# Kernel optimization log

Measured on AMD Instinct MI355X. Metric: run time of the kernel, lower is better.

The kernel has to match this reference:

```python
import jax, jax.numpy as jnp
import numpy as np

ALPHA = 0.5
SMOOTH = 1e-05
ITERS = 10


def _max_pool3x3(x):
    # 3x3 max pool, stride 1, SAME padding on NCHW tensor
    return jax.lax.reduce_window(
        x, -jnp.inf, jax.lax.max,
        window_dimensions=(1, 1, 3, 3),
        window_strides=(1, 1, 1, 1),
        padding='SAME')


def _soft_erode(x):
    return -_max_pool3x3(-x)


def _soft_dilate(x):
    return _max_pool3x3(x)


def _soft_skeletonize(img, iterations=ITERS):
    def body(skel, _):
        eroded = _soft_erode(skel)
        temp = _soft_dilate(eroded)
        skel = skel - (skel - eroded) * temp
        skel = jnp.clip(skel, 0.0, 1.0)
        return skel, None
    skel, _ = jax.lax.scan(body, img, None, length=iterations)
    return skel


def _dice_score(pred, target, smooth=SMOOTH):
    inter = jnp.sum(pred * target, axis=(2, 3))
    union = jnp.sum(pred, axis=(2, 3)) + jnp.sum(target, axis=(2, 3))
    dice = (2.0 * inter + smooth) / (union + smooth)
    return jnp.mean(dice)


def setup_inputs() -> dict:
    key = jax.random.key(0)
    k1, k2 = jax.random.split(key)
    B, C, H, W = 32, 1, 512, 512
    pred_logits = jax.random.normal(k1, (B, C, H, W), dtype=jnp.float32)
    target = jax.random.uniform(k2, (B, C, H, W), dtype=jnp.float32)
    return {"pred_logits": pred_logits, "target": target}


def reference(pred_logits, target):
    pred = jax.nn.sigmoid(pred_logits)
    dice = _dice_score(pred, target)
    pred_skel = _soft_skeletonize(pred)
    target_skel = _soft_skeletonize(target)
    skel_dice = _dice_score(pred_skel, target_skel)
    loss = (1.0 - ALPHA) * (1.0 - dice) + ALPHA * (1.0 - skel_dice)
    return (loss, dice, skel_dice)
```

## Files before the change

kernel.cpp:

```cpp
#include <hip/hip_runtime.h>
#include <hip/hip_fp16.h>
#include <math.h>


#define H 512
#define W 512
#define IMG (H * W)
#define NIMG 64
#define NPRED 32

#define APU 72
#define AROWS 74
#define BPU 68
#define BROWS 68
#define TQ 17
#define S1ITEMS 238
#define FILLN (AROWS * 18)

#define PINF2 0x7C007C00u
#define NINF2 0xFC00FC00u
#define ONE2  0x3C003C00u

typedef _Float16 f16;
typedef _Float16 h2 __attribute__((ext_vector_type(2)));
typedef __fp16 fp16v2 __attribute__((ext_vector_type(2)));

__device__ __forceinline__ float2 unpack2(uint u) {
    fp16v2 h = __builtin_bit_cast(fp16v2, u);
    return make_float2((float)h.x, (float)h.y);
}
__device__ __forceinline__ uint pack2(float a, float b) {
    fp16v2 h = __builtin_amdgcn_cvt_pkrtz(a, b);
    return __builtin_bit_cast(uint, h);
}
__device__ __forceinline__ uint pmin(uint a, uint b) {
    uint d; asm("v_pk_min_f16 %0, %1, %2" : "=v"(d) : "v"(a), "v"(b)); return d;
}
__device__ __forceinline__ uint pmax(uint a, uint b) {
    uint d; asm("v_pk_max_f16 %0, %1, %2" : "=v"(d) : "v"(a), "v"(b)); return d;
}
__device__ __forceinline__ uint abit(uint hi, uint lo) {
    return __builtin_amdgcn_alignbit(hi, lo, 16);
}

__device__ __forceinline__ void lds_dma16(uint* l, const void* g) {
    __builtin_amdgcn_global_load_lds(
        (__attribute__((address_space(1))) void*)(g),
        (__attribute__((address_space(3))) void*)(l), 16, 0, 0);
}

__device__ __forceinline__ float wsum64(float v) {
#pragma unroll
    for (int o = 32; o > 0; o >>= 1) v += __shfl_down(v, o);
    return v;
}

__device__ __forceinline__ void hmin8p(const uint* __restrict__ p, uint m[6], uint sc[4]) {
    uint4 w0 = *(const uint4*)(p);
    uint4 w1 = *(const uint4*)(p + 4);
    uint w[8] = {w0.x, w0.y, w0.z, w0.w, w1.x, w1.y, w1.z, w1.w};
    sc[0] = w[2]; sc[1] = w[3]; sc[2] = w[4]; sc[3] = w[5];
    uint s[7];
#pragma unroll
    for (int j = 0; j < 7; j++) s[j] = abit(w[j + 1], w[j]);
#pragma unroll
    for (int i = 0; i < 6; i++) m[i] = pmin(s[i], pmin(w[i + 1], s[i + 1]));
}

template<bool EDGE>
__device__ __forceinline__ void erode8(const uint a[6], const uint b[6], const uint c[6],
                                       bool rowok, const bool* eok, uint e[6]) {
#pragma unroll
    for (int i = 0; i < 6; i++) {
        uint v = pmin(a[i], pmin(b[i], c[i]));
        e[i] = EDGE ? ((rowok && eok[i]) ? v : NINF2) : v;
    }
}

__device__ __forceinline__ void hmax8(const uint e[6], uint hx[4], uint ec[4]) {
    uint a[5];
#pragma unroll
    for (int j = 0; j < 5; j++) a[j] = abit(e[j + 1], e[j]);
#pragma unroll
    for (int p = 0; p < 4; p++) {
        hx[p] = pmax(a[p], pmax(e[p + 1], a[p + 1]));
        ec[p] = e[p + 1];
    }
}

__device__ __forceinline__ uint upd_pair(uint s, uint ec, uint t) {
    h2 sh = __builtin_bit_cast(h2, s);
    h2 eh = __builtin_bit_cast(h2, ec);
    h2 th = __builtin_bit_cast(h2, t);
    h2 o = sh - (sh - eh) * th;
    return pmin(pmax(__builtin_bit_cast(uint, o), 0u), ONE2);
}

template<bool EDGE, int SIG>
__device__ float2 fillA_f32(uint* __restrict__ A, const float* __restrict__ src,
                            const float* __restrict__ tgt,
                            int tileX, int tileY, int tid) {
    float a = 0.0f, b = 0.0f;
#pragma unroll
    for (int hf = 0; hf < 2; hf++) {
        float4 v0[3], v1[3], t0[3], t1[3];
        bool ld[3];
#pragma unroll
        for (int j = 0; j < 3; j++) {
            const int i = tid + 256 * (3 * hf + j);
            const int r = i / 18;
            const int q = i - 18 * r;
            const int gy = tileY + r - 4;
            const int gx = tileX - 8 + 8 * q;
            bool ok = (i < FILLN);
            if (EDGE) ok = ok && (r < 72) && ((unsigned)gy < (unsigned)H) &&
                           ((unsigned)gx < (unsigned)W);
            ld[j] = ok;
            if (ok) {
                const float* sp = src + (size_t)gy * W + gx;
                v0[j] = *(const float4*)(sp);
                v1[j] = *(const float4*)(sp + 4);
                if (SIG) {
                    const float* tp = tgt + (size_t)gy * W + gx;
                    t0[j] = *(const float4*)(tp);
                    t1[j] = *(const float4*)(tp + 4);
                }
            }
        }
#pragma unroll
        for (int j = 0; j < 3; j++) {
            const int i = tid + 256 * (3 * hf + j);
            const int r = i / 18;
            const int q = i - 18 * r;
            if (i < FILLN) {
                uint4 w = make_uint4(PINF2, PINF2, PINF2, PINF2);
                if (ld[j]) {
                    float4 f0 = v0[j], f1 = v1[j];
                    if (SIG) {
                        f0.x = 1.0f / (1.0f + __expf(-f0.x));
                        f0.y = 1.0f / (1.0f + __expf(-f0.y));
                        f0.z = 1.0f / (1.0f + __expf(-f0.z));
                        f0.w = 1.0f / (1.0f + __expf(-f0.w));
                        f1.x = 1.0f / (1.0f + __expf(-f1.x));
                        f1.y = 1.0f / (1.0f + __expf(-f1.y));
                        f1.z = 1.0f / (1.0f + __expf(-f1.z));
                        f1.w = 1.0f / (1.0f + __expf(-f1.w));
                    }
                    if (((unsigned)(r - 4) < 64u) && ((unsigned)(q - 1) < 16u)) {
                        if (SIG) {
                            a += f0.x * t0[j].x + f0.y * t0[j].y + f0.z * t0[j].z +
                                 f0.w * t0[j].w + f1.x * t1[j].x + f1.y * t1[j].y +
                                 f1.z * t1[j].z + f1.w * t1[j].w;
                            b += f0.x + f0.y + f0.z + f0.w + f1.x + f1.y + f1.z + f1.w;
                        } else {
                            a += f0.x + f0.y + f0.z + f0.w + f1.x + f1.y + f1.z + f1.w;
                        }
                    }
                    w.x = pack2(f0.x, f0.y); w.y = pack2(f0.z, f0.w);
                    w.z = pack2(f1.x, f1.y); w.w = pack2(f1.z, f1.w);
                }
                *(uint4*)(A + r * APU + 4 * q) = w;
            }
        }
    }
    return make_float2(a, b);
}

__device__ __forceinline__ void fill_dma(uint* __restrict__ A, const f16* __restrict__ src,
                                         int tileX, int tileY, int tid) {
#pragma unroll
    for (int j = 0; j < 6; j++) {
        const int i = tid + 256 * j;
        if (i < FILLN) {
            const int r = i / 18;
            const int q = i - 18 * r;
            const int gy = tileY + r - 4;
            const int gx = tileX - 8 + 8 * q;
            if (gx < 0 || gx >= W) {
                *(uint4*)(A + 4 * i) = make_uint4(PINF2, PINF2, PINF2, PINF2);
            } else {
                const int gyc = min(max(gy, 0), H - 1);
                lds_dma16(A + 4 * i, src + (size_t)gyc * W + gx);
            }
        }
    }
}

template<bool EDGE>
__device__ void stage1(const uint* __restrict__ Au, uint* __restrict__ Bu,
                       int tileX, int tileY, int tid) {
    if (tid >= S1ITEMS) return;
    const int s = tid / TQ;
    const int g = tid - TQ * s;
    const int gcb = tileX + 8 * g - 4;
    const int ys = tileY - 2 + 5 * s;
    bool eok[6], wok[4];
    if (EDGE) {
#pragma unroll
        for (int i = 0; i < 6; i++) eok[i] = ((unsigned)(gcb - 2 + 2 * i) < (unsigned)W);
#pragma unroll
        for (int p = 0; p < 4; p++) wok[p] = ((unsigned)(gcb + 2 * p) < (unsigned)W);
    }
    const int lr = 5 * s + 2;
    const uint* Ab = Au + 4 * g;
    uint m[3][6], sc[3][4], hx[3][4], e[6], ec_cur[4], ec_nxt[4], tsc[4];
    hmin8p(Ab + (lr - 2) * APU, m[0], tsc);
    hmin8p(Ab + (lr - 1) * APU, m[1], tsc);
    hmin8p(Ab + (lr + 0) * APU, m[2], sc[0]);
    erode8<EDGE>(m[0], m[1], m[2], (unsigned)(ys - 1) < (unsigned)H, eok, e);
    hmax8(e, hx[0], ec_nxt);
    hmin8p(Ab + (lr + 1) * APU, m[0], sc[1]);
    erode8<EDGE>(m[1], m[2], m[0], (unsigned)ys < (unsigned)H, eok, e);
    hmax8(e, hx[1], ec_cur);
#pragma unroll
    for (int k = 0; k < 5; k++) {
        hmin8p(Ab + (lr + 2 + k) * APU, m[(k + 1) % 3], sc[(2 + k) % 3]);
        erode8<EDGE>(m[(k + 2) % 3], m[k % 3], m[(k + 1) % 3],
                     (unsigned)(ys + k + 1) < (unsigned)H, eok, e);
        hmax8(e, hx[(k + 2) % 3], ec_nxt);
        const int br = 5 * s + k;
        if (br < BROWS) {
            const bool rin = EDGE ? ((unsigned)(ys + k) < (unsigned)H) : true;
            uint o[4];
#pragma unroll
            for (int p = 0; p < 4; p++) {
                uint t = pmax(hx[k % 3][p], pmax(hx[(k + 1) % 3][p], hx[(k + 2) % 3][p]));
                uint v = upd_pair(sc[k % 3][p], ec_cur[p], t);
                o[p] = EDGE ? ((rin && wok[p]) ? v : PINF2) : v;
            }
            *(uint4*)(Bu + br * BPU + 4 * g) = make_uint4(o[0], o[1], o[2], o[3]);
        }
#pragma unroll
        for (int p = 0; p < 4; p++) ec_cur[p] = ec_nxt[p];
    }
}

template<bool EDGE, bool TOREG>
__device__ void stage2(const uint* __restrict__ Bu, int tileX, int tileY, int tid,
                       f16* __restrict__ gdst, uint* __restrict__ oreg) {
    const int g = tid & 15;
    const int ty = tid >> 4;
    const int X = tileX + 8 * g;
    const int gy0 = tileY + 4 * ty;
    const int rb = 4 * ty + 2;
    bool eok[6];
    if (EDGE) {
#pragma unroll
        for (int i = 0; i < 6; i++) eok[i] = ((unsigned)(X - 2 + 2 * i) < (unsigned)W);
    }
    const uint* Bb = Bu + 4 * g;
    uint m[3][6], sc[3][4], hx[3][4], e[6], ec_cur[4], ec_nxt[4], tsc[4];
    hmin8p(Bb + (rb - 2) * BPU, m[0], tsc);
    hmin8p(Bb + (rb - 1) * BPU, m[1], tsc);
    hmin8p(Bb + (rb + 0) * BPU, m[2], sc[0]);
    erode8<EDGE>(m[0], m[1], m[2], (unsigned)(gy0 - 1) < (unsigned)H, eok, e);
    hmax8(e, hx[0], ec_nxt);
    hmin8p(Bb + (rb + 1) * BPU, m[0], sc[1]);
    erode8<EDGE>(m[1], m[2], m[0], true, eok, e);
    hmax8(e, hx[1], ec_cur);
#pragma unroll
    for (int k = 0; k < 4; k++) {
        hmin8p(Bb + (rb + 2 + k) * BPU, m[(k + 1) % 3], sc[(2 + k) % 3]);
        erode8<EDGE>(m[(k + 2) % 3], m[k % 3], m[(k + 1) % 3],
                     (unsigned)(gy0 + k + 1) < (unsigned)H, eok, e);
        hmax8(e, hx[(k + 2) % 3], ec_nxt);
        uint o[4];
#pragma unroll
        for (int p = 0; p < 4; p++) {
            uint t = pmax(hx[k % 3][p], pmax(hx[(k + 1) % 3][p], hx[(k + 2) % 3][p]));
            o[p] = upd_pair(sc[k % 3][p], ec_cur[p], t);
        }
        if (TOREG) {
#pragma unroll
            for (int p = 0; p < 4; p++) oreg[4 * k + p] = o[p];
        } else {
            *(uint4*)(gdst + (size_t)(gy0 + k) * W + X) = make_uint4(o[0], o[1], o[2], o[3]);
        }
#pragma unroll
        for (int p = 0; p < 4; p++) ec_cur[p] = ec_nxt[p];
    }
}

__device__ __forceinline__ bool is_edge() {
    return (blockIdx.x == 0) | (blockIdx.x == 3) | (blockIdx.y == 0) | (blockIdx.y == 7);
}

__global__ __launch_bounds__(256, 4) void k_first(
    const float* __restrict__ logits, const float* __restrict__ target,
    f16* __restrict__ outb, float* __restrict__ parts0, float* __restrict__ parts1) {
    __shared__ __align__(16) uint A[AROWS * APU];
    __shared__ __align__(16) uint Bu[BROWS * BPU];
    __shared__ float red[8];
    const int img = blockIdx.z;
    const int tileX = blockIdx.x * 128, tileY = blockIdx.y * 64;
    const int tid = threadIdx.x;
    const bool pred = (img < NPRED);
    const bool edge = is_edge();
    float2 ab;
    if (edge) {
        if (pred) ab = fillA_f32<true, 1>(A, logits + (size_t)img * IMG,
                                          target + (size_t)img * IMG, tileX, tileY, tid);
        else      ab = fillA_f32<true, 0>(A, target + (size_t)(img - NPRED) * IMG,
                                          nullptr, tileX, tileY, tid);
    } else {
        if (pred) ab = fillA_f32<false, 1>(A, logits + (size_t)img * IMG,
                                           target + (size_t)img * IMG, tileX, tileY, tid);
        else      ab = fillA_f32<false, 0>(A, target + (size_t)(img - NPRED) * IMG,
                                           nullptr, tileX, tileY, tid);
    }
    __syncthreads();
    float a = wsum64(ab.x), b = wsum64(ab.y);
    if ((tid & 63) == 0) { red[tid >> 6] = a; red[4 + (tid >> 6)] = b; }
    if (edge) stage1<true>(A, Bu, tileX, tileY, tid);
    else      stage1<false>(A, Bu, tileX, tileY, tid);
    __syncthreads();
    if (tid == 0) {
        int bi = blockIdx.z * 32 + blockIdx.y * 4 + blockIdx.x;
        parts0[bi] = red[0] + red[1] + red[2] + red[3];
        parts1[bi] = red[4] + red[5] + red[6] + red[7];
    }
    if (edge) stage2<true, false>(Bu, tileX, tileY, tid, outb + (size_t)img * IMG, nullptr);
    else      stage2<false, false>(Bu, tileX, tileY, tid, outb + (size_t)img * IMG, nullptr);
}

__global__ __launch_bounds__(256, 4) void k_mid(
    const f16* __restrict__ in, f16* __restrict__ outb) {
    __shared__ __align__(16) uint A[AROWS * APU];
    __shared__ __align__(16) uint Bu[BROWS * BPU];
    const int img = blockIdx.z;
    const int tileX = blockIdx.x * 128, tileY = blockIdx.y * 64;
    const int tid = threadIdx.x;
    const bool edge = is_edge();
    fill_dma(A, in + (size_t)img * IMG, tileX, tileY, tid);
    __syncthreads();
    if (edge) {
        stage1<true>(A, Bu, tileX, tileY, tid);
        __syncthreads();
        stage2<true, false>(Bu, tileX, tileY, tid, outb + (size_t)img * IMG, nullptr);
    } else {
        stage1<false>(A, Bu, tileX, tileY, tid);
        __syncthreads();
        stage2<false, false>(Bu, tileX, tileY, tid, outb + (size_t)img * IMG, nullptr);
    }
}

__global__ __launch_bounds__(256, 4) void k_last(
    const f16* __restrict__ in, float* __restrict__ pA,
    float* __restrict__ pB, float* __restrict__ pC) {
    __shared__ __align__(16) uint A[AROWS * APU];
    __shared__ __align__(16) uint Bu[BROWS * BPU];
    __shared__ float red[12];
    const int img = blockIdx.z;
    const int tileX = blockIdx.x * 128, tileY = blockIdx.y * 64;
    const int tid = threadIdx.x;
    const bool edge = is_edge();
    uint op[16], ot[16];
    fill_dma(A, in + (size_t)img * IMG, tileX, tileY, tid);
    __syncthreads();
    if (edge) {
        stage1<true>(A, Bu, tileX, tileY, tid);
        __syncthreads();
        stage2<true, true>(Bu, tileX, tileY, tid, nullptr, op);
        fill_dma(A, in + (size_t)(img + NPRED) * IMG, tileX, tileY, tid);
        __syncthreads();
        stage1<true>(A, Bu, tileX, tileY, tid);
        __syncthreads();
        stage2<true, true>(Bu, tileX, tileY, tid, nullptr, ot);
    } else {
        stage1<false>(A, Bu, tileX, tileY, tid);
        __syncthreads();
        stage2<false, true>(Bu, tileX, tileY, tid, nullptr, op);
        fill_dma(A, in + (size_t)(img + NPRED) * IMG, tileX, tileY, tid);
        __syncthreads();
        stage1<false>(A, Bu, tileX, tileY, tid);
        __syncthreads();
        stage2<false, true>(Bu, tileX, tileY, tid, nullptr, ot);
    }
    float a = 0.0f, b = 0.0f, c = 0.0f;
#pragma unroll
    for (int j = 0; j < 16; j++) {
        float2 p = unpack2(op[j]);
        float2 t = unpack2(ot[j]);
        a += p.x * t.x + p.y * t.y;
        b += p.x + p.y;
        c += t.x + t.y;
    }
    a = wsum64(a); b = wsum64(b); c = wsum64(c);
    if ((tid & 63) == 0) {
        red[tid >> 6] = a; red[4 + (tid >> 6)] = b; red[8 + (tid >> 6)] = c;
    }
    __syncthreads();
    if (tid == 0) {
        int bi = img * 32 + blockIdx.y * 4 + blockIdx.x;
        pA[bi] = red[0] + red[1] + red[2] + red[3];
        pB[bi] = red[4] + red[5] + red[6] + red[7];
        pC[bi] = red[8] + red[9] + red[10] + red[11];
    }
}

__global__ __launch_bounds__(64) void finalize_img(
    const float* __restrict__ parts0, const float* __restrict__ parts1,
    const float* __restrict__ pA, const float* __restrict__ pB,
    const float* __restrict__ pC, float* __restrict__ dices) {
    const int i = blockIdx.x, t = threadIdx.x;
    const bool v = (t < 32);
    float inter = wsum64(v ? parts0[i * 32 + t] : 0.0f);
    float sp = wsum64(v ? parts1[i * 32 + t] : 0.0f);
    float st = wsum64(v ? parts0[(NPRED + i) * 32 + t] : 0.0f);
    float i2 = wsum64(v ? pA[i * 32 + t] : 0.0f);
    float sp2 = wsum64(v ? pB[i * 32 + t] : 0.0f);
    float st2 = wsum64(v ? pC[i * 32 + t] : 0.0f);
    if (t == 0) {
        dices[i] = (float)((2.0 * (double)inter + 1e-5) / ((double)sp + (double)st + 1e-5));
        dices[32 + i] = (float)((2.0 * (double)i2 + 1e-5) / ((double)sp2 + (double)st2 + 1e-5));
    }
}

__global__ void finalize_out(const float* __restrict__ dices, float* __restrict__ out) {
    const int t = threadIdx.x;
    double d = 0.0, sd = 0.0;
    if (t < 32) { d = dices[t]; sd = dices[32 + t]; }
#pragma unroll
    for (int o = 32; o > 0; o >>= 1) { d += __shfl_down(d, o); sd += __shfl_down(sd, o); }
    if (t == 0) {
        d *= (1.0 / 32.0); sd *= (1.0 / 32.0);
        out[0] = (float)(0.5 * (1.0 - d) + 0.5 * (1.0 - sd));
        out[1] = (float)d;
        out[2] = (float)sd;
    }
}

extern "C" void kernel_launch(void* const* d_in, const int* in_sizes, int n_in,
                              void* d_out, int out_size, void* d_ws, size_t ws_size,
                              hipStream_t stream) {
    (void)in_sizes; (void)n_in; (void)out_size; (void)ws_size;
    const float* logits = (const float*)d_in[0];
    const float* target = (const float*)d_in[1];
    float* out = (float*)d_out;
    f16* buf0 = (f16*)d_ws;
    f16* buf1 = buf0 + (size_t)NIMG * IMG;
    float* parts0 = (float*)(buf1 + (size_t)NIMG * IMG);
    float* parts1 = parts0 + 2048;
    float* pA = parts1 + 2048;
    float* pB = pA + 1024;
    float* pC = pB + 1024;
    float* dices = pC + 1024;

    dim3 blk(256, 1, 1);
    k_first<<<dim3(4, 8, NIMG), blk, 0, stream>>>(logits, target, buf0, parts0, parts1);
    k_mid<<<dim3(4, 8, NIMG), blk, 0, stream>>>(buf0, buf1);
    k_mid<<<dim3(4, 8, NIMG), blk, 0, stream>>>(buf1, buf0);
    k_mid<<<dim3(4, 8, NIMG), blk, 0, stream>>>(buf0, buf1);
    k_last<<<dim3(4, 8, NPRED), blk, 0, stream>>>(buf1, pA, pB, pC);
    finalize_img<<<32, 64, 0, stream>>>(parts0, parts1, pA, pB, pC, dices);
    finalize_out<<<1, 64, 0, stream>>>(dices, out);
}
```

Before: 220.0 us.

## Process two row tiles per k_mid block and overlap next DMA fill with stage2

k_mid now handles two vertically adjacent tiles per block, with the grid halved in y. The second tile's shared-memory fill is issued before the first tile's stage2 so the load overlaps compute. k_last likewise prefetches the target image's tile during the pred tile's stage2. This is meant to hide global load latency, at the cost of fewer blocks (less parallelism) in k_mid and a dependence on fill_dma being asynchronous with respect to stage2's reads of Bu only.

```diff
diff --git a/kernel.cpp b/kernel.cpp
--- a/kernel.cpp
+++ b/kernel.cpp
@@ -281,10 +281,6 @@
     }
 }
 
-__device__ __forceinline__ bool is_edge() {
-    return (blockIdx.x == 0) | (blockIdx.x == 3) | (blockIdx.y == 0) | (blockIdx.y == 7);
-}
-
 __global__ __launch_bounds__(256, 4) void k_first(
     const float* __restrict__ logits, const float* __restrict__ target,
     f16* __restrict__ outb, float* __restrict__ parts0, float* __restrict__ parts1) {
@@ -295,7 +291,8 @@
     const int tileX = blockIdx.x * 128, tileY = blockIdx.y * 64;
     const int tid = threadIdx.x;
     const bool pred = (img < NPRED);
-    const bool edge = is_edge();
+    const bool edge = (blockIdx.x == 0) | (blockIdx.x == 3) |
+                      (blockIdx.y == 0) | (blockIdx.y == 7);
     float2 ab;
     if (edge) {
         if (pred) ab = fillA_f32<true, 1>(A, logits + (size_t)img * IMG,
@@ -328,20 +325,30 @@
     __shared__ __align__(16) uint A[AROWS * APU];
     __shared__ __align__(16) uint Bu[BROWS * BPU];
     const int img = blockIdx.z;
-    const int tileX = blockIdx.x * 128, tileY = blockIdx.y * 64;
+    const int tileX = blockIdx.x * 128;
+    const int by0 = blockIdx.y * 2;
+    const int tY0 = by0 * 64, tY1 = tY0 + 64;
     const int tid = threadIdx.x;
-    const bool edge = is_edge();
-    fill_dma(A, in + (size_t)img * IMG, tileX, tileY, tid);
-    __syncthreads();
-    if (edge) {
-        stage1<true>(A, Bu, tileX, tileY, tid);
-        __syncthreads();
-        stage2<true, false>(Bu, tileX, tileY, tid, outb + (size_t)img * IMG, nullptr);
-    } else {
-        stage1<false>(A, Bu, tileX, tileY, tid);
-        __syncthreads();
-        stage2<false, false>(Bu, tileX, tileY, tid, outb + (size_t)img * IMG, nullptr);
-    }
+    const f16* src = in + (size_t)img * IMG;
+    f16* dst = outb + (size_t)img * IMG;
+    const bool ex = (blockIdx.x == 0) | (blockIdx.x == 3);
+    const bool e0 = ex | (by0 == 0);
+    const bool e1 = ex | (by0 + 1 == 7);
+
+    fill_dma(A, src, tileX, tY0, tid);
+    __syncthreads();
+    if (e0) stage1<true>(A, Bu, tileX, tY0, tid);
+    else    stage1<false>(A, Bu, tileX, tY0, tid);
+    __syncthreads();
+    fill_dma(A, src, tileX, tY1, tid);
+    if (e0) stage2<true, false>(Bu, tileX, tY0, tid, dst, nullptr);
+    else    stage2<false, false>(Bu, tileX, tY0, tid, dst, nullptr);
+    __syncthreads();
+    if (e1) stage1<true>(A, Bu, tileX, tY1, tid);
+    else    stage1<false>(A, Bu, tileX, tY1, tid);
+    __syncthreads();
+    if (e1) stage2<true, false>(Bu, tileX, tY1, tid, dst, nullptr);
+    else    stage2<false, false>(Bu, tileX, tY1, tid, dst, nullptr);
 }
 
 __global__ __launch_bounds__(256, 4) void k_last(
@@ -353,29 +360,23 @@
     const int img = blockIdx.z;
     const int tileX = blockIdx.x * 128, tileY = blockIdx.y * 64;
     const int tid = threadIdx.x;
-    const bool edge = is_edge();
+    const bool edge = (blockIdx.x == 0) | (blockIdx.x == 3) |
+                      (blockIdx.y == 0) | (blockIdx.y == 7);
     uint op[16], ot[16];
     fill_dma(A, in + (size_t)img * IMG, tileX, tileY, tid);
     __syncthreads();
-    if (edge) {
-        stage1<true>(A, Bu, tileX, tileY, tid);
-        __syncthreads();
-        stage2<true, true>(Bu, tileX, tileY, tid, nullptr, op);
-        fill_dma(A, in + (size_t)(img + NPRED) * IMG, tileX, tileY, tid);
-        __syncthreads();
-        stage1<true>(A, Bu, tileX, tileY, tid);
-        __syncthreads();
-        stage2<true, true>(Bu, tileX, tileY, tid, nullptr, ot);
-    } else {
-        stage1<false>(A, Bu, tileX, tileY, tid);
-        __syncthreads();
-        stage2<false, true>(Bu, tileX, tileY, tid, nullptr, op);
-        fill_dma(A, in + (size_t)(img + NPRED) * IMG, tileX, tileY, tid);
-        __syncthreads();
-        stage1<false>(A, Bu, tileX, tileY, tid);
-        __syncthreads();
-        stage2<false, true>(Bu, tileX, tileY, tid, nullptr, ot);
-    }
+    if (edge) stage1<true>(A, Bu, tileX, tileY, tid);
+    else      stage1<false>(A, Bu, tileX, tileY, tid);
+    __syncthreads();
+    fill_dma(A, in + (size_t)(img + NPRED) * IMG, tileX, tileY, tid);
+    if (edge) stage2<true, true>(Bu, tileX, tileY, tid, nullptr, op);
+    else      stage2<false, true>(Bu, tileX, tileY, tid, nullptr, op);
+    __syncthreads();
+    if (edge) stage1<true>(A, Bu, tileX, tileY, tid);
+    else      stage1<false>(A, Bu, tileX, tileY, tid);
+    __syncthreads();
+    if (edge) stage2<true, true>(Bu, tileX, tileY, tid, nullptr, ot);
+    else      stage2<false, true>(Bu, tileX, tileY, tid, nullptr, ot);
     float a = 0.0f, b = 0.0f, c = 0.0f;
 #pragma unroll
     for (int j = 0; j < 16; j++) {
@@ -448,9 +449,9 @@
 
     dim3 blk(256, 1, 1);
     k_first<<<dim3(4, 8, NIMG), blk, 0, stream>>>(logits, target, buf0, parts0, parts1);
-    k_mid<<<dim3(4, 8, NIMG), blk, 0, stream>>>(buf0, buf1);
-    k_mid<<<dim3(4, 8, NIMG), blk, 0, stream>>>(buf1, buf0);
-    k_mid<<<dim3(4, 8, NIMG), blk, 0, stream>>>(buf0, buf1);
+    k_mid<<<dim3(4, 4, NIMG), blk, 0, stream>>>(buf0, buf1);
+    k_mid<<<dim3(4, 4, NIMG), blk, 0, stream>>>(buf1, buf0);
+    k_mid<<<dim3(4, 4, NIMG), blk, 0, stream>>>(buf0, buf1);
     k_last<<<dim3(4, 8, NPRED), blk, 0, stream>>>(buf1, pA, pB, pC);
     finalize_img<<<32, 64, 0, stream>>>(parts0, parts1, pA, pB, pC, dices);
     finalize_out<<<1, 64, 0, stream>>>(dices, out);
```

Measured after the change: 222.7 us. Within noise of the previous version (+1.2%).

## Fuse four skeletonize iterations per kernel with wider halo tiles

Applied to the files above, without the earlier changes.

Replaces the three two-iteration mid kernels and the two-iteration last kernel with kernels that each run four skeleton iterations in shared memory. They use a wider halo (8 rows and 16 columns) and ping-pong between two LDS buffers. This removes two kernel launches and their global f16 round trips, at the cost of redundant halo compute, more LDS per block and lower occupancy (launch bounds 3). The last kernel also prefetches the target tile into LDS during the final stage of the pred chain.

```diff
diff --git a/kernel.cpp b/kernel.cpp
--- a/kernel.cpp
+++ b/kernel.cpp
@@ -11,11 +11,13 @@
 
 #define APU 72
 #define AROWS 74
-#define BPU 68
-#define BROWS 68
-#define TQ 17
-#define S1ITEMS 238
 #define FILLN (AROWS * 18)
+#define DPU 68
+#define A4P 80
+#define A4R 82
+#define B4P 76
+#define C4P 72
+#define FILL4N 1600
 
 #define PINF2 0x7C007C00u
 #define NINF2 0xFC00FC00u
@@ -94,6 +96,101 @@
     h2 th = __builtin_bit_cast(h2, t);
     h2 o = sh - (sh - eh) * th;
     return pmin(pmax(__builtin_bit_cast(uint, o), 0u), ONE2);
+}
+
+template<bool EDGE, int PIN, int POUT, int NG, int NSTRIP, int SROWS, int NROWS, int RO>
+__device__ void stageN(const uint* __restrict__ in, uint* __restrict__ out,
+                       int tileX, int tileY, int tid) {
+    if (tid >= NSTRIP * NG) return;
+    const int s = tid / NG;
+    const int g = tid - NG * s;
+    const int c0 = tileX - 2 * RO + 8 * g;
+    const int ys = tileY + SROWS * s - RO;
+    bool eok[6], wok[4];
+    if (EDGE) {
+#pragma unroll
+        for (int i = 0; i < 6; i++) eok[i] = ((unsigned)(c0 - 2 + 2 * i) < (unsigned)W);
+#pragma unroll
+        for (int p = 0; p < 4; p++) wok[p] = ((unsigned)(c0 + 2 * p) < (unsigned)W);
+    }
+    const int lr = SROWS * s + 2;
+    const uint* Ab = in + 4 * g;
+    uint m[3][6], sc[3][4], hx[3][4], e[6], ec_cur[4], ec_nxt[4], tsc[4];
+    hmin8p(Ab + (lr - 2) * PIN, m[0], tsc);
+    hmin8p(Ab + (lr - 1) * PIN, m[1], tsc);
+    hmin8p(Ab + (lr + 0) * PIN, m[2], sc[0]);
+    erode8<EDGE>(m[0], m[1], m[2], (unsigned)(ys - 1) < (unsigned)H, eok, e);
+    hmax8(e, hx[0], ec_nxt);
+    hmin8p(Ab + (lr + 1) * PIN, m[0], sc[1]);
+    erode8<EDGE>(m[1], m[2], m[0], (unsigned)ys < (unsigned)H, eok, e);
+    hmax8(e, hx[1], ec_cur);
+#pragma unroll
+    for (int k = 0; k < SROWS; k++) {
+        hmin8p(Ab + (lr + 2 + k) * PIN, m[(k + 1) % 3], sc[(2 + k) % 3]);
+        erode8<EDGE>(m[(k + 2) % 3], m[k % 3], m[(k + 1) % 3],
+                     (unsigned)(ys + k + 1) < (unsigned)H, eok, e);
+        hmax8(e, hx[(k + 2) % 3], ec_nxt);
+        const int br = SROWS * s + k;
+        if (NSTRIP * SROWS <= NROWS || br < NROWS) {
+            const bool rin = EDGE ? ((unsigned)(ys + k) < (unsigned)H) : true;
+            uint o[4];
+#pragma unroll
+            for (int p = 0; p < 4; p++) {
+                uint t = pmax(hx[k % 3][p], pmax(hx[(k + 1) % 3][p], hx[(k + 2) % 3][p]));
+                uint v = upd_pair(sc[k % 3][p], ec_cur[p], t);
+                o[p] = EDGE ? ((rin && wok[p]) ? v : PINF2) : v;
+            }
+            *(uint4*)(out + br * POUT + 4 * g) = make_uint4(o[0], o[1], o[2], o[3]);
+        }
+#pragma unroll
+        for (int p = 0; p < 4; p++) ec_cur[p] = ec_nxt[p];
+    }
+}
+
+template<bool EDGE, bool TOREG>
+__device__ void stage2(const uint* __restrict__ Du, int tileX, int tileY, int tid,
+                       f16* __restrict__ gdst, uint* __restrict__ oreg) {
+    const int g = tid & 15;
+    const int ty = tid >> 4;
+    const int X = tileX + 8 * g;
+    const int gy0 = tileY + 4 * ty;
+    const int rb = 4 * ty + 2;
+    bool eok[6];
+    if (EDGE) {
+#pragma unroll
+        for (int i = 0; i < 6; i++) eok[i] = ((unsigned)(X - 2 + 2 * i) < (unsigned)W);
+    }
+    const uint* Bb = Du + 4 * g;
+    uint m[3][6], sc[3][4], hx[3][4], e[6], ec_cur[4], ec_nxt[4], tsc[4];
+    hmin8p(Bb + (rb - 2) * DPU, m[0], tsc);
+    hmin8p(Bb + (rb - 1) * DPU, m[1], tsc);
+    hmin8p(Bb + (rb + 0) * DPU, m[2], sc[0]);
+    erode8<EDGE>(m[0], m[1], m[2], (unsigned)(gy0 - 1) < (unsigned)H, eok, e);
+    hmax8(e, hx[0], ec_nxt);
+    hmin8p(Bb + (rb + 1) * DPU, m[0], sc[1]);
+    erode8<EDGE>(m[1], m[2], m[0], true, eok, e);
+    hmax8(e, hx[1], ec_cur);
+#pragma unroll
+    for (int k = 0; k < 4; k++) {
+        hmin8p(Bb + (rb + 2 + k) * DPU, m[(k + 1) % 3], sc[(2 + k) % 3]);
+        erode8<EDGE>(m[(k + 2) % 3], m[k % 3], m[(k + 1) % 3],
+                     (unsigned)(gy0 + k + 1) < (unsigned)H, eok, e);
+        hmax8(e, hx[(k + 2) % 3], ec_nxt);
+        uint o[4];
+#pragma unroll
+        for (int p = 0; p < 4; p++) {
+            uint t = pmax(hx[k % 3][p], pmax(hx[(k + 1) % 3][p], hx[(k + 2) % 3][p]));
+            o[p] = upd_pair(sc[k % 3][p], ec_cur[p], t);
+        }
+        if (TOREG) {
+#pragma unroll
+            for (int p = 0; p < 4; p++) oreg[4 * k + p] = o[p];
+        } else {
+            *(uint4*)(gdst + (size_t)(gy0 + k) * W + X) = make_uint4(o[0], o[1], o[2], o[3]);
+        }
+#pragma unroll
+        for (int p = 0; p < 4; p++) ec_cur[p] = ec_nxt[p];
+    }
 }
 
 template<bool EDGE, int SIG>
@@ -166,119 +263,39 @@
     return make_float2(a, b);
 }
 
-__device__ __forceinline__ void fill_dma(uint* __restrict__ A, const f16* __restrict__ src,
-                                         int tileX, int tileY, int tid) {
-#pragma unroll
-    for (int j = 0; j < 6; j++) {
+__device__ __forceinline__ void fill_dma4(uint* __restrict__ A, const f16* __restrict__ src,
+                                          int tileX, int tileY, int tid) {
+#pragma unroll
+    for (int j = 0; j < 7; j++) {
         const int i = tid + 256 * j;
-        if (i < FILLN) {
-            const int r = i / 18;
-            const int q = i - 18 * r;
-            const int gy = tileY + r - 4;
-            const int gx = tileX - 8 + 8 * q;
+        if (i < FILL4N) {
+            const int r = i / 20;
+            const int q = i - 20 * r;
+            const int gy = tileY + r - 8;
+            const int gx = tileX - 16 + 8 * q;
             if (gx < 0 || gx >= W) {
-                *(uint4*)(A + 4 * i) = make_uint4(PINF2, PINF2, PINF2, PINF2);
+                *(uint4*)(A + r * A4P + 4 * q) = make_uint4(PINF2, PINF2, PINF2, PINF2);
             } else {
                 const int gyc = min(max(gy, 0), H - 1);
-                lds_dma16(A + 4 * i, src + (size_t)gyc * W + gx);
+                lds_dma16(A + r * A4P + 4 * q, src + (size_t)gyc * W + gx);
             }
         }
     }
 }
 
-template<bool EDGE>
-__device__ void stage1(const uint* __restrict__ Au, uint* __restrict__ Bu,
-                       int tileX, int tileY, int tid) {
-    if (tid >= S1ITEMS) return;
-    const int s = tid / TQ;
-    const int g = tid - TQ * s;
-    const int gcb = tileX + 8 * g - 4;
-    const int ys = tileY - 2 + 5 * s;
-    bool eok[6], wok[4];
-    if (EDGE) {
-#pragma unroll
-        for (int i = 0; i < 6; i++) eok[i] = ((unsigned)(gcb - 2 + 2 * i) < (unsigned)W);
-#pragma unroll
-        for (int p = 0; p < 4; p++) wok[p] = ((unsigned)(gcb + 2 * p) < (unsigned)W);
-    }
-    const int lr = 5 * s + 2;
-    const uint* Ab = Au + 4 * g;
-    uint m[3][6], sc[3][4], hx[3][4], e[6], ec_cur[4], ec_nxt[4], tsc[4];
-    hmin8p(Ab + (lr - 2) * APU, m[0], tsc);
-    hmin8p(Ab + (lr - 1) * APU, m[1], tsc);
-    hmin8p(Ab + (lr + 0) * APU, m[2], sc[0]);
-    erode8<EDGE>(m[0], m[1], m[2], (unsigned)(ys - 1) < (unsigned)H, eok, e);
-    hmax8(e, hx[0], ec_nxt);
-    hmin8p(Ab + (lr + 1) * APU, m[0], sc[1]);
-    erode8<EDGE>(m[1], m[2], m[0], (unsigned)ys < (unsigned)H, eok, e);
-    hmax8(e, hx[1], ec_cur);
-#pragma unroll
-    for (int k = 0; k < 5; k++) {
-        hmin8p(Ab + (lr + 2 + k) * APU, m[(k + 1) % 3], sc[(2 + k) % 3]);
-        erode8<EDGE>(m[(k + 2) % 3], m[k % 3], m[(k + 1) % 3],
-                     (unsigned)(ys + k + 1) < (unsigned)H, eok, e);
-        hmax8(e, hx[(k + 2) % 3], ec_nxt);
-        const int br = 5 * s + k;
-        if (br < BROWS) {
-            const bool rin = EDGE ? ((unsigned)(ys + k) < (unsigned)H) : true;
-            uint o[4];
-#pragma unroll
-            for (int p = 0; p < 4; p++) {
-                uint t = pmax(hx[k % 3][p], pmax(hx[(k + 1) % 3][p], hx[(k + 2) % 3][p]));
-                uint v = upd_pair(sc[k % 3][p], ec_cur[p], t);
-                o[p] = EDGE ? ((rin && wok[p]) ? v : PINF2) : v;
-            }
-            *(uint4*)(Bu + br * BPU + 4 * g) = make_uint4(o[0], o[1], o[2], o[3]);
-        }
-#pragma unroll
-        for (int p = 0; p < 4; p++) ec_cur[p] = ec_nxt[p];
-    }
-}
-
-template<bool EDGE, bool TOREG>
-__device__ void stage2(const uint* __restrict__ Bu, int tileX, int tileY, int tid,
-                       f16* __restrict__ gdst, uint* __restrict__ oreg) {
-    const int g = tid & 15;
-    const int ty = tid >> 4;
-    const int X = tileX + 8 * g;
-    const int gy0 = tileY + 4 * ty;
-    const int rb = 4 * ty + 2;
-    bool eok[6];
-    if (EDGE) {
-#pragma unroll
-        for (int i = 0; i < 6; i++) eok[i] = ((unsigned)(X - 2 + 2 * i) < (unsigned)W);
-    }
-    const uint* Bb = Bu + 4 * g;
-    uint m[3][6], sc[3][4], hx[3][4], e[6], ec_cur[4], ec_nxt[4], tsc[4];
-    hmin8p(Bb + (rb - 2) * BPU, m[0], tsc);
-    hmin8p(Bb + (rb - 1) * BPU, m[1], tsc);
-    hmin8p(Bb + (rb + 0) * BPU, m[2], sc[0]);
-    erode8<EDGE>(m[0], m[1], m[2], (unsigned)(gy0 - 1) < (unsigned)H, eok, e);
-    hmax8(e, hx[0], ec_nxt);
-    hmin8p(Bb + (rb + 1) * BPU, m[0], sc[1]);
-    erode8<EDGE>(m[1], m[2], m[0], true, eok, e);
-    hmax8(e, hx[1], ec_cur);
-#pragma unroll
-    for (int k = 0; k < 4; k++) {
-        hmin8p(Bb + (rb + 2 + k) * BPU, m[(k + 1) % 3], sc[(2 + k) % 3]);
-        erode8<EDGE>(m[(k + 2) % 3], m[k % 3], m[(k + 1) % 3],
-                     (unsigned)(gy0 + k + 1) < (unsigned)H, eok, e);
-        hmax8(e, hx[(k + 2) % 3], ec_nxt);
-        uint o[4];
-#pragma unroll
-        for (int p = 0; p < 4; p++) {
-            uint t = pmax(hx[k % 3][p], pmax(hx[(k + 1) % 3][p], hx[(k + 2) % 3][p]));
-            o[p] = upd_pair(sc[k % 3][p], ec_cur[p], t);
-        }
-        if (TOREG) {
-#pragma unroll
-            for (int p = 0; p < 4; p++) oreg[4 * k + p] = o[p];
-        } else {
-            *(uint4*)(gdst + (size_t)(gy0 + k) * W + X) = make_uint4(o[0], o[1], o[2], o[3]);
-        }
-#pragma unroll
-        for (int p = 0; p < 4; p++) ec_cur[p] = ec_nxt[p];
-    }
+template<bool EDGE, bool TOREG, bool PRE>
+__device__ void chain4(uint* __restrict__ A4, uint* __restrict__ B4,
+                       int tileX, int tileY, int tid,
+                       f16* __restrict__ dst, uint* __restrict__ oreg,
+                       const f16* __restrict__ pre) {
+    stageN<EDGE, A4P, B4P, 19, 13, 6, 76, 6>(A4, B4, tileX, tileY, tid);
+    __syncthreads();
+    stageN<EDGE, B4P, C4P, 18, 12, 6, 72, 4>(B4, A4, tileX, tileY, tid);
+    __syncthreads();
+    stageN<EDGE, C4P, DPU, 17, 14, 5, 68, 2>(A4, B4, tileX, tileY, tid);
+    __syncthreads();
+    if (PRE) fill_dma4(A4, pre, tileX, tileY, tid);
+    stage2<EDGE, TOREG>(B4, tileX, tileY, tid, dst, oreg);
 }
 
 __device__ __forceinline__ bool is_edge() {
@@ -289,7 +306,7 @@
     const float* __restrict__ logits, const float* __restrict__ target,
     f16* __restrict__ outb, float* __restrict__ parts0, float* __restrict__ parts1) {
     __shared__ __align__(16) uint A[AROWS * APU];
-    __shared__ __align__(16) uint Bu[BROWS * BPU];
+    __shared__ __align__(16) uint Bu[68 * DPU];
     __shared__ float red[8];
     const int img = blockIdx.z;
     const int tileX = blockIdx.x * 128, tileY = blockIdx.y * 64;
@@ -311,8 +328,8 @@
     __syncthreads();
     float a = wsum64(ab.x), b = wsum64(ab.y);
     if ((tid & 63) == 0) { red[tid >> 6] = a; red[4 + (tid >> 6)] = b; }
-    if (edge) stage1<true>(A, Bu, tileX, tileY, tid);
-    else      stage1<false>(A, Bu, tileX, tileY, tid);
+    if (edge) stageN<true, APU, DPU, 17, 14, 5, 68, 2>(A, Bu, tileX, tileY, tid);
+    else      stageN<false, APU, DPU, 17, 14, 5, 68, 2>(A, Bu, tileX, tileY, tid);
     __syncthreads();
     if (tid == 0) {
         int bi = blockIdx.z * 32 + blockIdx.y * 4 + blockIdx.x;
@@ -323,58 +340,44 @@
     else      stage2<false, false>(Bu, tileX, tileY, tid, outb + (size_t)img * IMG, nullptr);
 }
 
-__global__ __launch_bounds__(256, 4) void k_mid(
+__global__ __launch_bounds__(256, 3) void k_mid4(
     const f16* __restrict__ in, f16* __restrict__ outb) {
-    __shared__ __align__(16) uint A[AROWS * APU];
-    __shared__ __align__(16) uint Bu[BROWS * BPU];
+    __shared__ __align__(16) uint A4[A4R * A4P];
+    __shared__ __align__(16) uint B4[76 * B4P];
     const int img = blockIdx.z;
     const int tileX = blockIdx.x * 128, tileY = blockIdx.y * 64;
     const int tid = threadIdx.x;
     const bool edge = is_edge();
-    fill_dma(A, in + (size_t)img * IMG, tileX, tileY, tid);
-    __syncthreads();
-    if (edge) {
-        stage1<true>(A, Bu, tileX, tileY, tid);
-        __syncthreads();
-        stage2<true, false>(Bu, tileX, tileY, tid, outb + (size_t)img * IMG, nullptr);
-    } else {
-        stage1<false>(A, Bu, tileX, tileY, tid);
-        __syncthreads();
-        stage2<false, false>(Bu, tileX, tileY, tid, outb + (size_t)img * IMG, nullptr);
-    }
-}
-
-__global__ __launch_bounds__(256, 4) void k_last(
+    const f16* src = in + (size_t)img * IMG;
+    f16* dst = outb + (size_t)img * IMG;
+    fill_dma4(A4, src, tileX, tileY, tid);
+    __syncthreads();
+    if (edge) chain4<true, false, false>(A4, B4, tileX, tileY, tid, dst, nullptr, nullptr);
+    else      chain4<false, false, false>(A4, B4, tileX, tileY, tid, dst, nullptr, nullptr);
+}
+
+__global__ __launch_bounds__(256, 3) void k_last4(
     const f16* __restrict__ in, float* __restrict__ pA,
     float* __restrict__ pB, float* __restrict__ pC) {
-    __shared__ __align__(16) uint A[AROWS * APU];
-    __shared__ __align__(16) uint Bu[BROWS * BPU];
+    __shared__ __align__(16) uint A4[A4R * A4P];
+    __shared__ __align__(16) uint B4[76 * B4P];
     __shared__ float red[12];
     const int img = blockIdx.z;
     const int tileX = blockIdx.x * 128, tileY = blockIdx.y * 64;
     const int tid = threadIdx.x;
     const bool edge = is_edge();
     uint op[16], ot[16];
-    fill_dma(A, in + (size_t)img * IMG, tileX, tileY, tid);
+    const f16* tsrc = in + (size_t)(img + NPRED) * IMG;
+    fill_dma4(A4, in + (size_t)img * IMG, tileX, tileY, tid);
     __syncthreads();
     if (edge) {
-        stage1<true>(A, Bu, tileX, tileY, tid);
+        chain4<true, true, true>(A4, B4, tileX, tileY, tid, nullptr, op, tsrc);
         __syncthreads();
-        stage2<true, true>(Bu, tileX, tileY, tid, nullptr, op);
-        fill_dma(A, in + (size_t)(img + NPRED) * IMG, tileX, tileY, tid);
+        chain4<true, true, false>(A4, B4, tileX, tileY, tid, nullptr, ot, nullptr);
+    } else {
+        chain4<false, true, true>(A4, B4, tileX, tileY, tid, nullptr, op, tsrc);
         __syncthreads();
-        stage1<true>(A, Bu, tileX, tileY, tid);
-        __syncthreads();
-        stage2<true, true>(Bu, tileX, tileY, tid, nullptr, ot);
-    } else {
-        stage1<false>(A, Bu, tileX, tileY, tid);
-        __syncthreads();
-        stage2<false, true>(Bu, tileX, tileY, tid, nullptr, op);
-        fill_dma(A, in + (size_t)(img + NPRED) * IMG, tileX, tileY, tid);
-        __syncthreads();
-        stage1<false>(A, Bu, tileX, tileY, tid);
-        __syncthreads();
-        stage2<false, true>(Bu, tileX, tileY, tid, nullptr, ot);
+        chain4<false, true, false>(A4, B4, tileX, tileY, tid, nullptr, ot, nullptr);
     }
     float a = 0.0f, b = 0.0f, c = 0.0f;
 #pragma unroll
@@ -448,10 +451,8 @@
 
     dim3 blk(256, 1, 1);
     k_first<<<dim3(4, 8, NIMG), blk, 0, stream>>>(logits, target, buf0, parts0, parts1);
-    k_mid<<<dim3(4, 8, NIMG), blk, 0, stream>>>(buf0, buf1);
-    k_mid<<<dim3(4, 8, NIMG), blk, 0, stream>>>(buf1, buf0);
-    k_mid<<<dim3(4, 8, NIMG), blk, 0, stream>>>(buf0, buf1);
-    k_last<<<dim3(4, 8, NPRED), blk, 0, stream>>>(buf1, pA, pB, pC);
+    k_mid4<<<dim3(4, 8, NIMG), blk, 0, stream>>>(buf0, buf1);
+    k_last4<<<dim3(4, 8, NPRED), blk, 0, stream>>>(buf1, pA, pB, pC);
     finalize_img<<<32, 64, 0, stream>>>(parts0, parts1, pA, pB, pC, dices);
     finalize_out<<<1, 64, 0, stream>>>(dices, out);
 }
```

Result: no change. 220.9 us (+0.4%).
